# Performance work log

Measured on AMD Instinct MI355X. Metric: run time of the kernel, lower is better.

## Reference

```python
import jax, jax.numpy as jnp
import numpy as np


def setup_inputs() -> dict:
    key = jax.random.key(0)
    ks = jax.random.split(key, 9)
    B, N, E = 4, 100000, 400000
    Dv = De = Dc = 64
    Din, H, Dout = De + 2 * Dv + Dc, 128, 64  # 256, 128, 64
    return {
        "vdata": jax.random.normal(ks[0], (B, N, Dv), dtype=jnp.float32),
        "edata": jax.random.normal(ks[1], (B, E, De), dtype=jnp.float32),
        "cdata": jax.random.normal(ks[2], (B, Dc), dtype=jnp.float32),
        "W1": jax.random.normal(ks[3], (Din, H), dtype=jnp.float32) * (1.0 / np.sqrt(Din)),
        "b1": jnp.zeros((H,), dtype=jnp.float32),
        "W2": jax.random.normal(ks[4], (H, Dout), dtype=jnp.float32) * (1.0 / np.sqrt(H)),
        "b2": jnp.zeros((Dout,), dtype=jnp.float32),
        "sender_ids": jax.random.randint(ks[5], (B, E), 0, N, dtype=jnp.int64 if jax.config.jax_enable_x64 else jnp.int32).astype(jnp.int32),
        "receiver_ids": jax.random.randint(ks[6], (B, E), 0, N, dtype=jnp.int64 if jax.config.jax_enable_x64 else jnp.int32).astype(jnp.int32),
    }


def reference(vdata, edata, cdata, W1, b1, W2, b2, sender_ids, receiver_ids):
    # Gather sender/receiver vertex features per edge: [B,E,Dv]
    gather = jax.vmap(lambda v, idx: v[idx])  # per-graph gather along node dim
    sender_data = gather(vdata, sender_ids)
    receiver_data = gather(vdata, receiver_ids)
    B, E = edata.shape[0], edata.shape[1]
    # Context repeated per edge: [B,E,Dc]
    ctx = jnp.broadcast_to(cdata[:, None, :], (B, E, cdata.shape[-1]))
    # etin = cat(edge, sender, receiver, context) along feature dim -> [B,E,256]
    etin = jnp.concatenate([edata, sender_data, receiver_data, ctx], axis=2)
    # Batched MLP updater
    h = jax.nn.relu(jnp.einsum("bei,ih->beh", etin, W1) + b1)
    out = jnp.einsum("beh,ho->beo", h, W2) + b2
    return out
```

## Files before the change

kernel.cpp:

```cpp
#include <hip/hip_runtime.h>

typedef __attribute__((ext_vector_type(8))) __bf16 bf16x8;
typedef __attribute__((ext_vector_type(4))) float f32x4;
typedef __attribute__((ext_vector_type(4))) unsigned int u32x4;

#define NV 100000
#define NE 400000
#define NT (NE / 32)

#define VTAB_ELEMS ((size_t)4 * NV * 64)
#define VTAB_BYTES (VTAB_ELEMS * 2)
#define WS_NEED (VTAB_BYTES + 2048)

#define W1T_OFF 0
#define W2T_OFF 49152
#define LDS_SIZE 65536

__device__ inline unsigned short f2b_rne(float f) {
    unsigned u = __builtin_bit_cast(unsigned, f);
    return (unsigned short)((u + 0x7fffu + ((u >> 16) & 1u)) >> 16);
}

__device__ inline unsigned pk2(float lo, float hi) {
    unsigned r;
    asm("v_cvt_pk_bf16_f32 %0, %1, %2" : "=v"(r) : "v"(lo), "v"(hi));
    return r;
}

__device__ inline bf16x8 pack8(f32x4 a, f32x4 b) {
    u32x4 u = {pk2(a[0], a[1]), pk2(a[2], a[3]), pk2(b[0], b[1]), pk2(b[2], b[3])};
    return __builtin_bit_cast(bf16x8, u);
}

__device__ inline f32x4 ldv(const float* p) { return *(const f32x4*)p; }
__device__ inline f32x4 ntl(const float* p) { return __builtin_nontemporal_load((const f32x4*)p); }

__device__ inline bf16x8 load8(const float* p) {
    f32x4 x = *(const f32x4*)p;
    f32x4 y = *(const f32x4*)(p + 4);
    return pack8(x, y);
}

__global__ __launch_bounds__(256) void vconv_kernel(const float* __restrict__ vdata,
                                                    unsigned short* __restrict__ vt)
{
    const size_t G = VTAB_ELEMS / 8;
    for (size_t g = (size_t)blockIdx.x * blockDim.x + threadIdx.x; g < G;
         g += (size_t)gridDim.x * blockDim.x) {
        const float* p = vdata + g * 8;
        *(bf16x8*)(vt + g * 8) = pack8(ldv(p), ldv(p + 4));
    }
}

__global__ __launch_bounds__(512) void hc_kernel(const float* __restrict__ W1,
                                                 const float* __restrict__ b1,
                                                 const float* __restrict__ cdata,
                                                 float* __restrict__ hc)
{
    const int tid = threadIdx.x;
    const int b = tid >> 7, hid = tid & 127;
    float s = b1[hid];
#pragma unroll 8
    for (int j = 0; j < 64; ++j)
        s += cdata[b * 64 + j] * W1[(192 + j) * 128 + hid];
    hc[b * 128 + hid] = s;
}

__global__ __launch_bounds__(512, 4) void edgeblock_kernel(
    const unsigned short* __restrict__ vt, const float* __restrict__ hc,
    const float* __restrict__ edata, const float* __restrict__ W1,
    const float* __restrict__ W2, const float* __restrict__ b2,
    const int* __restrict__ snd, const int* __restrict__ rcv,
    float* __restrict__ out)
{
    __shared__ __align__(16) unsigned char lds[LDS_SIZE];
    const int tid = threadIdx.x;
    const int lane = tid & 63;
    const int w = tid >> 6;
    const int l15 = lane & 15;
    const int lg = lane >> 4;

    const int bid = blockIdx.x;
    const int xcd = bid & 7;
    const int b   = xcd >> 1;
    const int blk = ((bid >> 3) << 1) | (xcd & 1);

    for (int i = tid; i < 192 * 128; i += 512) {
        int k = i >> 7, n = i & 127;
        *(unsigned short*)(lds + W1T_OFF + n * 384 + ((k * 2) ^ ((n & 7) << 4))) = f2b_rne(W1[i]);
    }
    for (int i = tid; i < 128 * 64; i += 512) {
        int k = i >> 6, n = i & 63;
        int kc2 = k >> 5, c = k & 31;
        int j   = ((c >> 4) << 2) | (c & 3);
        int lgs = (c >> 2) & 3;
        int off = kc2 * 64 + lgs * 16 + j * 2;
        *(unsigned short*)(lds + W2T_OFF + n * 256 + (off ^ ((n & 7) << 4))) = f2b_rne(W2[i]);
    }
    __syncthreads();

    const size_t bE = (size_t)b * NE;
    const float* ed_b = edata + bE * 64;
    const unsigned short* vt_b = vt + (size_t)b * NV * 64;
    const float* hc_b = hc + b * 128;
    const int* snd_b = snd + bE;
    const int* rcv_b = rcv + bE;
    float* out_b = out + bE * 64;

    for (int t = blk * 8 + w; t < NT; t += 1024) {
        const int e0 = t * 32;
        const int sid0 = snd_b[e0 + l15], sid1 = snd_b[e0 + 16 + l15];
        const int rid0 = rcv_b[e0 + l15], rid1 = rcv_b[e0 + 16 + l15];

        const float* er0 = ed_b + (size_t)(e0 + l15) * 64 + lg * 8;
        const float* er1 = er0 + 16 * 64;

        bf16x8 af[6][2];
        af[0][0] = pack8(ntl(er0), ntl(er0 + 4));
        af[0][1] = pack8(ntl(er1), ntl(er1 + 4));
        af[1][0] = pack8(ntl(er0 + 32), ntl(er0 + 36));
        af[1][1] = pack8(ntl(er1 + 32), ntl(er1 + 36));
        {
            const unsigned short* s0 = vt_b + (size_t)sid0 * 64 + lg * 8;
            const unsigned short* s1 = vt_b + (size_t)sid1 * 64 + lg * 8;
            const unsigned short* r0 = vt_b + (size_t)rid0 * 64 + lg * 8;
            const unsigned short* r1 = vt_b + (size_t)rid1 * 64 + lg * 8;
            af[2][0] = *(const bf16x8*)(s0);      af[2][1] = *(const bf16x8*)(s1);
            af[3][0] = *(const bf16x8*)(s0 + 32); af[3][1] = *(const bf16x8*)(s1 + 32);
            af[4][0] = *(const bf16x8*)(r0);      af[4][1] = *(const bf16x8*)(r1);
            af[5][0] = *(const bf16x8*)(r0 + 32); af[5][1] = *(const bf16x8*)(r1 + 32);
        }

        f32x4 acc1[8][2];
#pragma unroll
        for (int ht = 0; ht < 8; ++ht) {
            f32x4 bv = ldv(hc_b + ht * 16 + lg * 4);
            acc1[ht][0] = bv; acc1[ht][1] = bv;
        }

#pragma unroll
        for (int kc = 0; kc < 6; ++kc) {
            const bf16x8 bc0 = af[kc][0];
            const bf16x8 bc1 = af[kc][1];
#pragma unroll
            for (int ht = 0; ht < 8; ++ht) {
                const int row = ht * 16 + l15;
                const bf16x8 wf = *(const bf16x8*)(lds + W1T_OFF + row * 384 +
                                                   ((kc * 64 + lg * 16) ^ ((row & 7) << 4)));
                acc1[ht][0] = __builtin_amdgcn_mfma_f32_16x16x32_bf16(wf, bc0, acc1[ht][0], 0, 0, 0);
                acc1[ht][1] = __builtin_amdgcn_mfma_f32_16x16x32_bf16(wf, bc1, acc1[ht][1], 0, 0, 0);
            }
        }

        bf16x8 q[2][4];
#pragma unroll
        for (int kc2 = 0; kc2 < 4; ++kc2)
#pragma unroll
            for (int et = 0; et < 2; ++et) {
                f32x4 u = acc1[2 * kc2][et], v = acc1[2 * kc2 + 1][et];
                u32x4 pq;
                pq[0] = pk2(fmaxf(u[0], 0.f), fmaxf(u[1], 0.f));
                pq[1] = pk2(fmaxf(u[2], 0.f), fmaxf(u[3], 0.f));
                pq[2] = pk2(fmaxf(v[0], 0.f), fmaxf(v[1], 0.f));
                pq[3] = pk2(fmaxf(v[2], 0.f), fmaxf(v[3], 0.f));
                q[et][kc2] = __builtin_bit_cast(bf16x8, pq);
            }

        f32x4 acc2[4][2];
#pragma unroll
        for (int dt = 0; dt < 4; ++dt) {
            f32x4 bv = ldv(b2 + dt * 16 + lg * 4);
            acc2[dt][0] = bv; acc2[dt][1] = bv;
        }
#pragma unroll
        for (int kc2 = 0; kc2 < 4; ++kc2)
#pragma unroll
            for (int dt = 0; dt < 4; ++dt) {
                const int row = dt * 16 + l15;
                const bf16x8 wf = *(const bf16x8*)(lds + W2T_OFF + row * 256 +
                                                   ((kc2 * 64 + lg * 16) ^ ((row & 7) << 4)));
                acc2[dt][0] = __builtin_amdgcn_mfma_f32_16x16x32_bf16(wf, q[0][kc2], acc2[dt][0], 0, 0, 0);
                acc2[dt][1] = __builtin_amdgcn_mfma_f32_16x16x32_bf16(wf, q[1][kc2], acc2[dt][1], 0, 0, 0);
            }

        float* ob0 = out_b + (size_t)(e0 + l15) * 64 + lg * 4;
        float* ob1 = ob0 + 16 * 64;
#pragma unroll
        for (int dt = 0; dt < 4; ++dt) {
            *(f32x4*)(ob0 + dt * 16) = acc2[dt][0];
            *(f32x4*)(ob1 + dt * 16) = acc2[dt][1];
        }
    }
}

__global__ __launch_bounds__(512, 4) void edgeblock_legacy(
    const float* __restrict__ vdata, const float* __restrict__ edata,
    const float* __restrict__ cdata, const float* __restrict__ W1,
    const float* __restrict__ b1, const float* __restrict__ W2,
    const float* __restrict__ b2, const int* __restrict__ snd,
    const int* __restrict__ rcv, float* __restrict__ out)
{
    __shared__ __align__(16) unsigned char lds[81920];
    const int tid = threadIdx.x;
    const int lane = tid & 63;
    const int w = tid >> 6;
    const int l15 = lane & 15;
    const int lg = lane >> 4;
    const int bid = blockIdx.x;
    const int xcd = bid & 7;
    const int b   = xcd >> 1;
    const int blk = ((bid >> 3) << 1) | (xcd & 1);

    for (int i = tid; i < 256 * 128; i += 512) {
        int k = i >> 7, n = i & 127;
        *(unsigned short*)(lds + n * 512 + ((k * 2) ^ ((n & 7) << 4))) = f2b_rne(W1[i]);
    }
    for (int i = tid; i < 128 * 64; i += 512) {
        int k = i >> 6, n = i & 63;
        int kc2 = k >> 5, c = k & 31;
        int j   = ((c >> 4) << 2) | (c & 3);
        int lgs = (c >> 2) & 3;
        int off = kc2 * 64 + lgs * 16 + j * 2;
        *(unsigned short*)(lds + 65536 + n * 256 + (off ^ ((n & 7) << 4))) = f2b_rne(W2[i]);
    }
    __syncthreads();

    const float* cd = cdata + b * 64;
    const bf16x8 cfr0 = load8(cd + lg * 8);
    const bf16x8 cfr1 = load8(cd + 32 + lg * 8);

    const size_t bE = (size_t)b * NE;
    const float* ed_b = edata + bE * 64;
    const float* vd_b = vdata + (size_t)b * NV * 64;
    const int* snd_b = snd + bE;
    const int* rcv_b = rcv + bE;
    float* out_b = out + bE * 64;

    for (int t = blk * 8 + w; t < NT; t += 1024) {
        const int e0 = t * 32;
        const int sid0 = snd_b[e0 + l15], sid1 = snd_b[e0 + 16 + l15];
        const int rid0 = rcv_b[e0 + l15], rid1 = rcv_b[e0 + 16 + l15];
        const float* er0 = ed_b + (size_t)(e0 + l15) * 64 + lg * 8;
        const float* er1 = er0 + 16 * 64;
        const float* sr0 = vd_b + (size_t)sid0 * 64 + lg * 8;
        const float* sr1 = vd_b + (size_t)sid1 * 64 + lg * 8;
        const float* rr0 = vd_b + (size_t)rid0 * 64 + lg * 8;
        const float* rr1 = vd_b + (size_t)rid1 * 64 + lg * 8;

        bf16x8 af[6][2];
        af[0][0] = load8(er0);      af[0][1] = load8(er1);
        af[1][0] = load8(er0 + 32); af[1][1] = load8(er1 + 32);
        af[2][0] = load8(sr0);      af[2][1] = load8(sr1);
        af[3][0] = load8(sr0 + 32); af[3][1] = load8(sr1 + 32);
        af[4][0] = load8(rr0);      af[4][1] = load8(rr1);
        af[5][0] = load8(rr0 + 32); af[5][1] = load8(rr1 + 32);

        f32x4 acc1[8][2];
#pragma unroll
        for (int ht = 0; ht < 8; ++ht) {
            f32x4 bv = ldv(b1 + ht * 16 + lg * 4);
            acc1[ht][0] = bv; acc1[ht][1] = bv;
        }
#pragma unroll
        for (int kc = 0; kc < 8; ++kc) {
            bf16x8 bc0, bc1;
            if (kc < 6)      { bc0 = af[kc][0]; bc1 = af[kc][1]; }
            else if (kc == 6){ bc0 = cfr0;      bc1 = cfr0; }
            else             { bc0 = cfr1;      bc1 = cfr1; }
#pragma unroll
            for (int ht = 0; ht < 8; ++ht) {
                const int row = ht * 16 + l15;
                const bf16x8 wf = *(const bf16x8*)(lds + row * 512 +
                                                   ((kc * 64 + lg * 16) ^ ((row & 7) << 4)));
                acc1[ht][0] = __builtin_amdgcn_mfma_f32_16x16x32_bf16(wf, bc0, acc1[ht][0], 0, 0, 0);
                acc1[ht][1] = __builtin_amdgcn_mfma_f32_16x16x32_bf16(wf, bc1, acc1[ht][1], 0, 0, 0);
            }
        }

        bf16x8 q[2][4];
#pragma unroll
        for (int kc2 = 0; kc2 < 4; ++kc2)
#pragma unroll
            for (int et = 0; et < 2; ++et) {
                f32x4 u = acc1[2 * kc2][et], v = acc1[2 * kc2 + 1][et];
                u32x4 pq;
                pq[0] = pk2(fmaxf(u[0], 0.f), fmaxf(u[1], 0.f));
                pq[1] = pk2(fmaxf(u[2], 0.f), fmaxf(u[3], 0.f));
                pq[2] = pk2(fmaxf(v[0], 0.f), fmaxf(v[1], 0.f));
                pq[3] = pk2(fmaxf(v[2], 0.f), fmaxf(v[3], 0.f));
                q[et][kc2] = __builtin_bit_cast(bf16x8, pq);
            }

        f32x4 acc2[4][2];
#pragma unroll
        for (int dt = 0; dt < 4; ++dt) {
            f32x4 bv = ldv(b2 + dt * 16 + lg * 4);
            acc2[dt][0] = bv; acc2[dt][1] = bv;
        }
#pragma unroll
        for (int kc2 = 0; kc2 < 4; ++kc2)
#pragma unroll
            for (int dt = 0; dt < 4; ++dt) {
                const int row = dt * 16 + l15;
                const bf16x8 wf = *(const bf16x8*)(lds + 65536 + row * 256 +
                                                   ((kc2 * 64 + lg * 16) ^ ((row & 7) << 4)));
                acc2[dt][0] = __builtin_amdgcn_mfma_f32_16x16x32_bf16(wf, q[0][kc2], acc2[dt][0], 0, 0, 0);
                acc2[dt][1] = __builtin_amdgcn_mfma_f32_16x16x32_bf16(wf, q[1][kc2], acc2[dt][1], 0, 0, 0);
            }

        float* ob0 = out_b + (size_t)(e0 + l15) * 64 + lg * 4;
        float* ob1 = ob0 + 16 * 64;
#pragma unroll
        for (int dt = 0; dt < 4; ++dt) {
            *(f32x4*)(ob0 + dt * 16) = acc2[dt][0];
            *(f32x4*)(ob1 + dt * 16) = acc2[dt][1];
        }
    }
}

extern "C" void kernel_launch(void* const* d_in, const int* in_sizes, int n_in,
                              void* d_out, int out_size, void* d_ws, size_t ws_size,
                              hipStream_t stream) {
    const float* vdata = (const float*)d_in[0];
    const float* edata = (const float*)d_in[1];
    const float* cdata = (const float*)d_in[2];
    const float* W1    = (const float*)d_in[3];
    const float* b1    = (const float*)d_in[4];
    const float* W2    = (const float*)d_in[5];
    const float* b2    = (const float*)d_in[6];
    const int*   snd   = (const int*)d_in[7];
    const int*   rcv   = (const int*)d_in[8];
    float* out = (float*)d_out;

    if (ws_size >= WS_NEED) {
        unsigned short* vt = (unsigned short*)d_ws;
        float* hc = (float*)((char*)d_ws + VTAB_BYTES);
        vconv_kernel<<<dim3(2048), dim3(256), 0, stream>>>(vdata, vt);
        hc_kernel<<<dim3(1), dim3(512), 0, stream>>>(W1, b1, cdata, hc);
        edgeblock_kernel<<<dim3(512), dim3(512), 0, stream>>>(
            vt, hc, edata, W1, W2, b2, snd, rcv, out);
    } else {
        edgeblock_legacy<<<dim3(512), dim3(512), 0, stream>>>(
            vdata, edata, cdata, W1, b1, W2, b2, snd, rcv, out);
    }
}
```

Measured before the change: 324.7 us.

## Software-pipeline vertex gathers one tile ahead of the MLP compute

Restructures the per-wave edge-tile loop so that the sender/receiver indices and bf16 vertex-feature gathers for the next tile are issued during the current tile's layer-1/layer-2 MFMA work. This aims to hide the latency of random vertex gathers behind compute. It costs extra registers for the double-buffered gather fragments, which could hurt occupancy under the 512x4 launch bound. It also assumes every block has at least one tile, since the first gather is unconditional.

```diff
diff --git a/kernel.cpp b/kernel.cpp
--- a/kernel.cpp
+++ b/kernel.cpp
@@ -65,6 +65,27 @@
         s += cdata[b * 64 + j] * W1[(192 + j) * 128 + hid];
     hc[b * 128 + hid] = s;
 }
+
+
+#define VT_GATHER(S0, S1, R0, R1, d20, d21, d30, d31, d40, d41, d50, d51) { \
+    const unsigned short* s0_ = vt_b + (size_t)(S0) * 64 + lg * 8; \
+    const unsigned short* s1_ = vt_b + (size_t)(S1) * 64 + lg * 8; \
+    const unsigned short* r0_ = vt_b + (size_t)(R0) * 64 + lg * 8; \
+    const unsigned short* r1_ = vt_b + (size_t)(R1) * 64 + lg * 8; \
+    d20 = *(const bf16x8*)(s0_);      d21 = *(const bf16x8*)(s1_); \
+    d30 = *(const bf16x8*)(s0_ + 32); d31 = *(const bf16x8*)(s1_ + 32); \
+    d40 = *(const bf16x8*)(r0_);      d41 = *(const bf16x8*)(r1_); \
+    d50 = *(const bf16x8*)(r0_ + 32); d51 = *(const bf16x8*)(r1_ + 32); }
+
+#define L1STEP(KC, BC0, BC1) { \
+    _Pragma("unroll") \
+    for (int ht = 0; ht < 8; ++ht) { \
+        const int row = ht * 16 + l15; \
+        const bf16x8 wf = *(const bf16x8*)(lds + W1T_OFF + row * 384 + \
+            (((KC) * 64 + lg * 16) ^ ((row & 7) << 4))); \
+        acc1[ht][0] = __builtin_amdgcn_mfma_f32_16x16x32_bf16(wf, BC0, acc1[ht][0], 0, 0, 0); \
+        acc1[ht][1] = __builtin_amdgcn_mfma_f32_16x16x32_bf16(wf, BC1, acc1[ht][1], 0, 0, 0); \
+    } }
 
 __global__ __launch_bounds__(512, 4) void edgeblock_kernel(
     const unsigned short* __restrict__ vt, const float* __restrict__ hc,
@@ -107,29 +128,35 @@
     const int* rcv_b = rcv + bE;
     float* out_b = out + bE * 64;
 
-    for (int t = blk * 8 + w; t < NT; t += 1024) {
+    int t = blk * 8 + w;
+
+    bf16x8 a20, a21, a30, a31, a40, a41, a50, a51;
+    {
         const int e0 = t * 32;
-        const int sid0 = snd_b[e0 + l15], sid1 = snd_b[e0 + 16 + l15];
-        const int rid0 = rcv_b[e0 + l15], rid1 = rcv_b[e0 + 16 + l15];
-
+        const int s0 = snd_b[e0 + l15], s1 = snd_b[e0 + 16 + l15];
+        const int r0 = rcv_b[e0 + l15], r1 = rcv_b[e0 + 16 + l15];
+        VT_GATHER(s0, s1, r0, r1, a20, a21, a30, a31, a40, a41, a50, a51);
+    }
+    int tn = t + 1024;
+    bool more = tn < NT;
+
+    for (;;) {
+        int nS0, nS1, nR0, nR1;
+        if (more) {
+            const int en = tn * 32;
+            nS0 = snd_b[en + l15]; nS1 = snd_b[en + 16 + l15];
+            nR0 = rcv_b[en + l15]; nR1 = rcv_b[en + 16 + l15];
+        }
+
+        const int e0 = t * 32;
         const float* er0 = ed_b + (size_t)(e0 + l15) * 64 + lg * 8;
         const float* er1 = er0 + 16 * 64;
-
-        bf16x8 af[6][2];
-        af[0][0] = pack8(ntl(er0), ntl(er0 + 4));
-        af[0][1] = pack8(ntl(er1), ntl(er1 + 4));
-        af[1][0] = pack8(ntl(er0 + 32), ntl(er0 + 36));
-        af[1][1] = pack8(ntl(er1 + 32), ntl(er1 + 36));
-        {
-            const unsigned short* s0 = vt_b + (size_t)sid0 * 64 + lg * 8;
-            const unsigned short* s1 = vt_b + (size_t)sid1 * 64 + lg * 8;
-            const unsigned short* r0 = vt_b + (size_t)rid0 * 64 + lg * 8;
-            const unsigned short* r1 = vt_b + (size_t)rid1 * 64 + lg * 8;
-            af[2][0] = *(const bf16x8*)(s0);      af[2][1] = *(const bf16x8*)(s1);
-            af[3][0] = *(const bf16x8*)(s0 + 32); af[3][1] = *(const bf16x8*)(s1 + 32);
-            af[4][0] = *(const bf16x8*)(r0);      af[4][1] = *(const bf16x8*)(r1);
-            af[5][0] = *(const bf16x8*)(r0 + 32); af[5][1] = *(const bf16x8*)(r1 + 32);
-        }
+        f32x4 g0 = ntl(er0),      g1 = ntl(er0 + 4);
+        f32x4 g2 = ntl(er1),      g3 = ntl(er1 + 4);
+        f32x4 g4 = ntl(er0 + 32), g5 = ntl(er0 + 36);
+        f32x4 g6 = ntl(er1 + 32), g7 = ntl(er1 + 36);
+        bf16x8 e00 = pack8(g0, g1), e01 = pack8(g2, g3);
+        bf16x8 e10 = pack8(g4, g5), e11 = pack8(g6, g7);
 
         f32x4 acc1[8][2];
 #pragma unroll
@@ -138,18 +165,16 @@
             acc1[ht][0] = bv; acc1[ht][1] = bv;
         }
 
-#pragma unroll
-        for (int kc = 0; kc < 6; ++kc) {
-            const bf16x8 bc0 = af[kc][0];
-            const bf16x8 bc1 = af[kc][1];
-#pragma unroll
-            for (int ht = 0; ht < 8; ++ht) {
-                const int row = ht * 16 + l15;
-                const bf16x8 wf = *(const bf16x8*)(lds + W1T_OFF + row * 384 +
-                                                   ((kc * 64 + lg * 16) ^ ((row & 7) << 4)));
-                acc1[ht][0] = __builtin_amdgcn_mfma_f32_16x16x32_bf16(wf, bc0, acc1[ht][0], 0, 0, 0);
-                acc1[ht][1] = __builtin_amdgcn_mfma_f32_16x16x32_bf16(wf, bc1, acc1[ht][1], 0, 0, 0);
-            }
+        L1STEP(0, e00, e01)
+        L1STEP(1, e10, e11)
+        L1STEP(2, a20, a21)
+        L1STEP(3, a30, a31)
+        L1STEP(4, a40, a41)
+        L1STEP(5, a50, a51)
+
+        bf16x8 b20, b21, b30, b31, b40, b41, b50, b51;
+        if (more) {
+            VT_GATHER(nS0, nS1, nR0, nR1, b20, b21, b30, b31, b40, b41, b50, b51);
         }
 
         bf16x8 q[2][4];
@@ -183,13 +208,20 @@
                 acc2[dt][1] = __builtin_amdgcn_mfma_f32_16x16x32_bf16(wf, q[1][kc2], acc2[dt][1], 0, 0, 0);
             }
 
-        float* ob0 = out_b + (size_t)(e0 + l15) * 64 + lg * 4;
-        float* ob1 = ob0 + 16 * 64;
-#pragma unroll
-        for (int dt = 0; dt < 4; ++dt) {
-            *(f32x4*)(ob0 + dt * 16) = acc2[dt][0];
-            *(f32x4*)(ob1 + dt * 16) = acc2[dt][1];
-        }
+        {
+            float* ob0 = out_b + (size_t)(e0 + l15) * 64 + lg * 4;
+            float* ob1 = ob0 + 16 * 64;
+#pragma unroll
+            for (int dt = 0; dt < 4; ++dt) {
+                *(f32x4*)(ob0 + dt * 16) = acc2[dt][0];
+                *(f32x4*)(ob1 + dt * 16) = acc2[dt][1];
+            }
+        }
+
+        if (!more) break;
+        a20 = b20; a21 = b21; a30 = b30; a31 = b31;
+        a40 = b40; a41 = b41; a50 = b50; a51 = b51;
+        t = tn; tn += 1024; more = tn < NT;
     }
 }
 
```

Result: slower. 400.3 us (+23.3%).
